# Performance work log

Hardware: AMD Instinct MI355X
Metric: run time of the kernel (lower is better)

## Reference

```python
import jax, jax.numpy as jnp
import numpy as np

B, N = 16, 4096
COORD, VAL = 2, 3
LD = 256          # latent_dim / code_dim
NC = 1024         # num_codes
HID = 256         # hidden_size
NL = 5            # num_layers
NV = 4            # num_latent_vectors (residual VQ stages)
NI = 1000         # num_images
CC = 0.25         # commitment_cost
OMEGA = 30.0


def setup_inputs() -> dict:
    key = jax.random.key(0)
    ks = jax.random.split(key, 12)
    coords = jax.random.uniform(ks[0], (B, N, COORD), jnp.float32, -1.0, 1.0)
    latent_indices = jax.random.randint(ks[1], (B,), 0, NI)
    latents = jax.random.normal(ks[2], (NI, NV, LD), jnp.float32)
    emb = jax.random.normal(ks[3], (NV, NC, LD), jnp.float32)
    emb = emb / jnp.linalg.norm(emb, axis=-1, keepdims=True)
    mod_W = jax.random.normal(ks[4], (NL, LD, 2 * HID), jnp.float32) * (1.0 / np.sqrt(LD))
    mod_b = jnp.zeros((NL, 2 * HID), jnp.float32)
    # SIREN init
    W0 = jax.random.uniform(ks[5], (COORD, HID), jnp.float32, -1.0 / COORD, 1.0 / COORD)
    b0 = jax.random.uniform(ks[6], (HID,), jnp.float32, -1.0 / np.sqrt(COORD), 1.0 / np.sqrt(COORD))
    w_bound = np.sqrt(6.0 / HID) / OMEGA
    Wh = jax.random.uniform(ks[7], (NL - 1, HID, HID), jnp.float32, -w_bound, w_bound)
    bh = jax.random.uniform(ks[8], (NL - 1, HID), jnp.float32, -1.0 / np.sqrt(HID), 1.0 / np.sqrt(HID))
    Wl = jax.random.uniform(ks[9], (HID, VAL), jnp.float32, -w_bound, w_bound)
    bl = jax.random.uniform(ks[10], (VAL,), jnp.float32, -1.0 / np.sqrt(HID), 1.0 / np.sqrt(HID))
    return {"coords": coords, "latent_indices": latent_indices, "latents": latents,
            "emb": emb, "mod_W": mod_W, "mod_b": mod_b, "W0": W0, "b0": b0,
            "Wh": Wh, "bh": bh, "Wl": Wl, "bl": bl}


def reference(coords, latent_indices, latents, emb, mod_W, mod_b, W0, b0, Wh, bh, Wl, bl):
    sg = jax.lax.stop_gradient
    # per-image latent, summed over latent vectors -> [B, LD]
    img_latents = latents[latent_indices]
    z = img_latents.sum(axis=1)
    residual = z
    z_q_sum = jnp.zeros_like(z)
    vq_loss = jnp.float32(0.0)
    for s in range(NV):  # fixed small residual-VQ stage loop
        E = emb[s]  # [NC, LD]
        # squared euclidean distances [B, NC]
        dist = (jnp.sum(residual ** 2, axis=1, keepdims=True)
                - 2.0 * residual @ E.T + jnp.sum(E ** 2, axis=1))
        idx = jnp.argmin(dist, axis=1)
        z_q = E[idx]  # [B, LD]
        z_q_st = residual + sg(z_q - residual)  # straight-through
        vq_loss = vq_loss + CC * jnp.mean((sg(z_q) - residual) ** 2)
        z_q_sum = z_q_sum + z_q_st
        residual = sg(residual - z_q_st)
    vq_loss = vq_loss / NV
    effective_z = z_q_sum  # eval: no warmup scaling
    # FiLM params per layer: [B, NL, 2*HID]
    mods = jnp.einsum('bd,ldh->blh', effective_z, mod_W) + mod_b
    gam, bet = jnp.split(mods, 2, axis=-1)  # each [B, NL, HID]
    # SIREN decoder, keeping [B, N, HID] layout
    x = jnp.sin(OMEGA * (coords @ W0 + b0))
    for i in range(1, NL):
        pre = x @ Wh[i - 1] + bh[i - 1]
        pre = pre * (1.0 + gam[:, i, None, :]) + bet[:, i, None, :]
        x = jnp.sin(OMEGA * pre)
    values = x @ Wl + bl  # [B, N, VAL]
    return values, vq_loss
```

## Files before the change

kernel.cpp:

```cpp
#include <hip/hip_runtime.h>
#include <math.h>

#define LDIM 256
#define NCODES 1024
#define HID 256
#define NLAY 5
#define NVQ 4
#define CC_ 0.25f
#define OMEGA_ 30.0f
#define BATCH 16
#define NPTS 4096
#define PTILE 64

#define WIN_OFF 4096
#define PART_OFF 4224
#define CNT_OFF 5280
#define FLAG_OFF 5288
#define FILM_OFF 8192
#define WP_BYTE 196608
#define PLANE_SHORTS (4 * 16 * 8 * 64 * 8)
#define FAST_WS_NEEDED 1245184u
#define MAGIC_ 0x13572468u

typedef __attribute__((ext_vector_type(8))) short short8;
typedef __attribute__((ext_vector_type(4))) float f32x4;

__device__ __forceinline__ unsigned int pack_split(float x) {
  unsigned int u = __builtin_bit_cast(unsigned int, x);
  float hf = __builtin_bit_cast(float, u & 0xffff0000u);
  float lf = x - hf;
  unsigned int ul = __builtin_bit_cast(unsigned int, lf);
  return (u & 0xffff0000u) | (ul >> 16);
}
__device__ __forceinline__ void split_trunc(float x, short& hi, short& lo) {
  unsigned int u = __builtin_bit_cast(unsigned int, x);
  float hf = __builtin_bit_cast(float, u & 0xffff0000u);
  float lf = x - hf;
  hi = (short)(u >> 16);
  lo = (short)(__builtin_bit_cast(unsigned int, lf) >> 16);
}
__device__ __forceinline__ float bf16_hi_f(unsigned short h) {
  return __builtin_bit_cast(float, (unsigned int)h << 16);
}
__device__ __forceinline__ unsigned int mono_u32(float f) {
  unsigned int u = __builtin_bit_cast(unsigned int, f);
  return (u & 0x80000000u) ? ~u : (u | 0x80000000u);
}

__global__ __launch_bounds__(256) void vq_prep_fused(
    const int* __restrict__ lidx,
    const float* __restrict__ latents,
    const float* __restrict__ emb,
    const float* __restrict__ Whg,
    float* __restrict__ ws, int do_prep) {
  const int blk = blockIdx.x;
  const int t = threadIdx.x;

  if (blk < 32) {
    if (!do_prep) return;
    const int li = blk >> 3;
    const int c  = blk & 7;
    const int lane = t & 63;
    const int n = lane & 15, q = lane >> 4;
    short* wp_hi = (short*)((char*)ws + WP_BYTE);
    short* wp_lo = wp_hi + PLANE_SHORTS;
    for (int h_t = (t >> 6); h_t < 16; h_t += 4) {
      short8 hv, lv;
      #pragma unroll
      for (int j = 0; j < 8; ++j) {
        float x = Whg[((size_t)(li * 256 + c * 32 + q * 8 + j)) * 256 + h_t * 16 + n];
        short hi, lo;
        split_trunc(x, hi, lo);
        hv[j] = hi; lv[j] = lo;
      }
      size_t off = ((((size_t)li * 16 + h_t) * 8 + c) * 64 + lane) * 8;
      *(short8*)&wp_hi[off] = hv;
      *(short8*)&wp_lo[off] = lv;
    }
    return;
  }

  __shared__ __align__(16) float Ech[32 * 260];
  __shared__ __align__(16) float r_s[LDIM];
  __shared__ float mval[256];
  __shared__ int   midx[256];
  __shared__ int   bcast;
  const int vqb = blk - 32;
  const int b = vqb >> 3;
  const int slice = vqb & 7;
  unsigned int* cnt  = (unsigned int*)(ws + CNT_OFF);
  unsigned int* flag = (unsigned int*)(ws + FLAG_OFF);
  unsigned long long* part = (unsigned long long*)(ws + PART_OFF);
  unsigned long long* winners = (unsigned long long*)(ws + WIN_OFF);

  if (vqb == 0 && t == 0) {
    #pragma unroll
    for (int i = 0; i < 8; ++i)
      __hip_atomic_store(&cnt[i], 0u, __ATOMIC_RELAXED, __HIP_MEMORY_SCOPE_AGENT);
    __hip_atomic_store(flag, MAGIC_, __ATOMIC_RELEASE, __HIP_MEMORY_SCOPE_AGENT);
  }

  const int ib = lidx[b];
  float z = 0.f;
  #pragma unroll
  for (int v = 0; v < NVQ; ++v) z += latents[((size_t)ib * NVQ + v) * LDIM + t];
  r_s[t] = z;
  if (slice == 0) ws[b * LDIM + t] = z;

  if (t == 0) {
    int guard = 0;
    while (__hip_atomic_load(flag, __ATOMIC_ACQUIRE, __HIP_MEMORY_SCOPE_AGENT) != MAGIC_
           && guard < (1 << 21)) { __builtin_amdgcn_s_sleep(8); ++guard; }
  }
  __syncthreads();

  const int cg = t >> 3;
  const int dq = t & 7;

  for (int s = 0; s < NVQ; ++s) {
    const float* E = emb + (size_t)s * NCODES * LDIM + (size_t)slice * 128 * LDIM;
    const float4* E4 = (const float4*)E;
    float bestv = 3.4e38f; int besti = 0;
    for (int ch = 0; ch < 4; ++ch) {
      __syncthreads();
      #pragma unroll
      for (int it = 0; it < 8; ++it) {
        int f = it * 256 + t;
        int row = f >> 6;
        int col4 = f & 63;
        *(float4*)&Ech[row * 260 + col4 * 4] = E4[(size_t)(ch * 32 + row) * 64 + col4];
      }
      __syncthreads();
      float dot = 0.f, e2 = 0.f;
      const float* er = &Ech[cg * 260];
      const float4* rr4 = (const float4*)r_s;
      #pragma unroll
      for (int j = 0; j < 8; ++j) {
        int d4 = dq + 8 * j;
        float4 e = *(const float4*)&er[d4 * 4];
        float4 rv = rr4[d4];
        dot += e.x * rv.x + e.y * rv.y + e.z * rv.z + e.w * rv.w;
        e2  += e.x * e.x + e.y * e.y + e.z * e.z + e.w * e.w;
      }
      dot += __shfl_xor(dot, 1); e2 += __shfl_xor(e2, 1);
      dot += __shfl_xor(dot, 2); e2 += __shfl_xor(e2, 2);
      dot += __shfl_xor(dot, 4); e2 += __shfl_xor(e2, 4);
      if (dq == 0) {
        float dist = e2 - 2.f * dot;
        int c = slice * 128 + ch * 32 + cg;
        if (dist < bestv) { bestv = dist; besti = c; }
      }
    }
    mval[t] = (dq == 0) ? bestv : 3.4e38f;
    midx[t] = (dq == 0) ? besti : (1 << 30);
    __syncthreads();
    for (int off = 128; off > 0; off >>= 1) {
      if (t < off) {
        float ov = mval[t + off]; int oi = midx[t + off];
        if (ov < mval[t] || (ov == mval[t] && oi < midx[t])) { mval[t] = ov; midx[t] = oi; }
      }
      __syncthreads();
    }
    if (t == 0) {
      unsigned long long pack =
          ((unsigned long long)mono_u32(mval[0]) << 32) | (unsigned int)midx[0];
      __hip_atomic_store(&part[(b * NVQ + s) * 8 + slice], pack,
                         __ATOMIC_RELAXED, __HIP_MEMORY_SCOPE_AGENT);
      __hip_atomic_fetch_add(&cnt[s], 1u, __ATOMIC_RELEASE, __HIP_MEMORY_SCOPE_AGENT);
      int guard = 0;
      while (__hip_atomic_load(&cnt[s], __ATOMIC_ACQUIRE, __HIP_MEMORY_SCOPE_AGENT) < 128u
             && guard < (1 << 21)) { __builtin_amdgcn_s_sleep(8); ++guard; }
      unsigned long long best =
          __hip_atomic_load(&part[(b * NVQ + s) * 8 + 0], __ATOMIC_RELAXED, __HIP_MEMORY_SCOPE_AGENT);
      #pragma unroll
      for (int s2 = 1; s2 < 8; ++s2) {
        unsigned long long v =
            __hip_atomic_load(&part[(b * NVQ + s) * 8 + s2], __ATOMIC_RELAXED, __HIP_MEMORY_SCOPE_AGENT);
        if (v < best) best = v;
      }
      bcast = (int)(best & 0xffffffffULL);
      if (slice == 0) winners[b * NVQ + s] = (unsigned long long)(unsigned int)bcast;
    }
    __syncthreads();
    const int w = bcast;
    r_s[t] -= emb[((size_t)s * NCODES + w) * LDIM + t];
    __syncthreads();
  }
}

__global__ __launch_bounds__(256) void film_loss(const float* __restrict__ emb,
                                                 const float* __restrict__ mod_W,
                                                 const float* __restrict__ mod_b,
                                                 float* __restrict__ ws,
                                                 float* __restrict__ loss_out) {
  __shared__ float z_s[LDIM];
  const int t = threadIdx.x;
  const unsigned long long* wsl = (const unsigned long long*)(ws + WIN_OFF);
  if (blockIdx.x == 64) {
    __shared__ float red[256];
    float acc = 0.f;
    for (int b = 0; b < BATCH; ++b) {
      float r = ws[b * LDIM + t];
      #pragma unroll
      for (int s = 0; s < NVQ; ++s) {
        int w = (int)(wsl[b * NVQ + s] & 0xffffffffULL);
        float e = emb[((size_t)s * NCODES + w) * LDIM + t];
        float d = e - r;
        acc += d * d;
        r -= e;
      }
    }
    red[t] = acc;
    __syncthreads();
    for (int off = 128; off > 0; off >>= 1) {
      if (t < off) red[t] += red[t + off];
      __syncthreads();
    }
    if (t == 0) loss_out[0] = red[0] * (CC_ / (NVQ * BATCH * LDIM));
    return;
  }
  const int li = blockIdx.x & 3;
  const int b  = blockIdx.x >> 2;
  const int l  = li + 1;
  float z = 0.f;
  #pragma unroll
  for (int s = 0; s < NVQ; ++s) {
    int w = (int)(wsl[b * NVQ + s] & 0xffffffffULL);
    z += emb[((size_t)s * NCODES + w) * LDIM + t];
  }
  z_s[t] = z;
  __syncthreads();
  float m1 = mod_b[l * 2 * HID + t];
  float m2 = mod_b[l * 2 * HID + HID + t];
  const float* Wm = mod_W + (size_t)l * LDIM * 2 * HID;
  #pragma unroll 4
  for (int d = 0; d < LDIM; ++d) {
    float zd = z_s[d];
    m1 = fmaf(zd, Wm[d * 2 * HID + t], m1);
    m2 = fmaf(zd, Wm[d * 2 * HID + HID + t], m2);
  }
  float* film = ws + FILM_OFF;
  film[((b * 4 + li) * 2 + 0) * HID + t] = 1.f + m1;
  film[((b * 4 + li) * 2 + 1) * HID + t] = m2;
}

__global__ __launch_bounds__(512) void siren_mfma_fast(
    const float* __restrict__ coords,
    const float* __restrict__ W0,
    const float* __restrict__ b0,
    const float* __restrict__ bhv,
    const float* __restrict__ Wl,
    const float* __restrict__ bl,
    const float* __restrict__ ws,
    float* __restrict__ out) {
  __shared__ short x_h[PTILE * 264];
  __shared__ short x_l[PTILE * 264];
  __shared__ float osum[PTILE * 8 * 3];
  const int tid = threadIdx.x;
  const int bp = blockIdx.x;
  const int b = bp >> 6;
  const int tile = bp & 63;
  const int pbase = b * NPTS + tile * PTILE;

  {
    const int oct = tid >> 6;
    const int p = tid & 63;
    const float c0 = coords[(size_t)(pbase + p) * 2 + 0];
    const float c1 = coords[(size_t)(pbase + p) * 2 + 1];
    const int d0 = oct * 32;
    for (int i = 0; i < 32; i += 8) {
      short8 hv, lv;
      #pragma unroll
      for (int j = 0; j < 8; ++j) {
        int d = d0 + i + j;
        float pre = fmaf(c0, W0[d], fmaf(c1, W0[HID + d], b0[d]));
        short hi, lo;
        split_trunc(__sinf(OMEGA_ * pre), hi, lo);
        hv[j] = hi; lv[j] = lo;
      }
      *(short8*)&x_h[p * 264 + d0 + i] = hv;
      *(short8*)&x_l[p * 264 + d0 + i] = lv;
    }
  }

  const int lane = tid & 63;
  const int hq = tid >> 6;
  const int hb = hq * 32;
  const int n = lane & 15;
  const int q = lane >> 4;

  const short* wp_hi = (const short*)((const char*)ws + WP_BYTE);
  const short* wp_lo = wp_hi + PLANE_SHORTS;
  const float* film = ws + FILM_OFF;

  for (int layer = 1; layer < NLAY; ++layer) {
    const int li = layer - 1;
    f32x4 acc[4][2];
    #pragma unroll
    for (int pt = 0; pt < 4; ++pt)
      #pragma unroll
      for (int ht = 0; ht < 2; ++ht)
        acc[pt][ht] = (f32x4){0.f, 0.f, 0.f, 0.f};

    __syncthreads();

    #pragma unroll 2
    for (int kc = 0; kc < HID; kc += 32) {
      const int c = kc >> 5;
      short8 Bh[2], Bl[2];
      #pragma unroll
      for (int ht = 0; ht < 2; ++ht) {
        const size_t wb = ((((size_t)li * 16 + hq * 2 + ht) * 8 + c) * 64 + lane) * 8;
        Bh[ht] = *(const short8*)&wp_hi[wb];
        Bl[ht] = *(const short8*)&wp_lo[wb];
      }
      short8 Ah[4], Al[4];
      #pragma unroll
      for (int pt = 0; pt < 4; ++pt) {
        const int xb = (pt * 16 + n) * 264 + kc + q * 8;
        Ah[pt] = *(const short8*)&x_h[xb];
        Al[pt] = *(const short8*)&x_l[xb];
      }
      #pragma unroll
      for (int ht = 0; ht < 2; ++ht)
        #pragma unroll
        for (int pt = 0; pt < 4; ++pt)
          acc[pt][ht] = __builtin_amdgcn_mfma_f32_16x16x32_bf16(Ah[pt], Bh[ht], acc[pt][ht], 0, 0, 0);
      #pragma unroll
      for (int ht = 0; ht < 2; ++ht)
        #pragma unroll
        for (int pt = 0; pt < 4; ++pt)
          acc[pt][ht] = __builtin_amdgcn_mfma_f32_16x16x32_bf16(Ah[pt], Bl[ht], acc[pt][ht], 0, 0, 0);
      #pragma unroll
      for (int ht = 0; ht < 2; ++ht)
        #pragma unroll
        for (int pt = 0; pt < 4; ++pt)
          acc[pt][ht] = __builtin_amdgcn_mfma_f32_16x16x32_bf16(Al[pt], Bh[ht], acc[pt][ht], 0, 0, 0);
    }

    __syncthreads();

    #pragma unroll
    for (int ht = 0; ht < 2; ++ht) {
      const int h = hb + ht * 16 + n;
      const float bias = bhv[li * HID + h];
      const float g1 = film[((b * 4 + li) * 2 + 0) * HID + h];
      const float bt = film[((b * 4 + li) * 2 + 1) * HID + h];
      #pragma unroll
      for (int pt = 0; pt < 4; ++pt) {
        #pragma unroll
        for (int r = 0; r < 4; ++r) {
          float pre = acc[pt][ht][r] + bias;
          pre = fmaf(pre, g1, bt);
          short hi, lo;
          split_trunc(__sinf(OMEGA_ * pre), hi, lo);
          const int row = pt * 16 + q * 4 + r;
          x_h[row * 264 + h] = hi;
          x_l[row * 264 + h] = lo;
        }
      }
    }
  }
  __syncthreads();

  {
    const int p = tid >> 3;
    const int dq = tid & 7;
    float v0 = 0.f, v1 = 0.f, v2 = 0.f;
    for (int i = 0; i < 32; ++i) {
      int d = dq * 32 + i;
      float xv = bf16_hi_f((unsigned short)x_h[p * 264 + d]) +
                 bf16_hi_f((unsigned short)x_l[p * 264 + d]);
      v0 = fmaf(xv, Wl[d * 3 + 0], v0);
      v1 = fmaf(xv, Wl[d * 3 + 1], v1);
      v2 = fmaf(xv, Wl[d * 3 + 2], v2);
    }
    osum[(p * 8 + dq) * 3 + 0] = v0;
    osum[(p * 8 + dq) * 3 + 1] = v1;
    osum[(p * 8 + dq) * 3 + 2] = v2;
  }
  __syncthreads();
  if (tid < PTILE) {
    const int p = tid;
    float v[3] = {bl[0], bl[1], bl[2]};
    #pragma unroll
    for (int dq = 0; dq < 8; ++dq)
      #pragma unroll
      for (int c = 0; c < 3; ++c) v[c] += osum[(p * 8 + dq) * 3 + c];
    size_t o = (size_t)(pbase + p) * 3;
    out[o + 0] = v[0]; out[o + 1] = v[1]; out[o + 2] = v[2];
  }
}

__global__ __launch_bounds__(512) void siren_mfma(
    const float* __restrict__ coords,
    const float* __restrict__ W0,
    const float* __restrict__ b0,
    const float* __restrict__ Whg,
    const float* __restrict__ bhv,
    const float* __restrict__ Wl,
    const float* __restrict__ bl,
    const float* __restrict__ ws,
    float* __restrict__ out) {
  __shared__ unsigned int x_u[128 * 260];
  __shared__ float osum[128 * 4 * 3];
  const int tid = threadIdx.x;
  const int bp = blockIdx.x;
  const int b = bp >> 5;
  const int tile = bp & 31;
  const int pbase = b * NPTS + tile * 128;
  {
    const int quarter = tid >> 7;
    const int p = tid & 127;
    const float c0 = coords[(size_t)(pbase + p) * 2 + 0];
    const float c1 = coords[(size_t)(pbase + p) * 2 + 1];
    const int d0 = quarter * 64;
    for (int i = 0; i < 64; i += 4) {
      unsigned int buf[4];
      #pragma unroll
      for (int j = 0; j < 4; ++j) {
        int d = d0 + i + j;
        float pre = fmaf(c0, W0[d], fmaf(c1, W0[HID + d], b0[d]));
        buf[j] = pack_split(__sinf(OMEGA_ * pre));
      }
      *(uint4*)&x_u[p * 260 + d0 + i] = *(uint4*)buf;
    }
  }
  const int lane = tid & 63;
  const int wv = tid >> 6;
  const int pg = wv & 1;
  const int hq = wv >> 1;
  const int pb = pg * 64;
  const int hb = hq * 64;
  const int n = lane & 15;
  const int q = lane >> 4;
  const float* film = ws + FILM_OFF;
  for (int layer = 1; layer < NLAY; ++layer) {
    const int li = layer - 1;
    f32x4 acc[4][4];
    #pragma unroll
    for (int pt = 0; pt < 4; ++pt)
      #pragma unroll
      for (int ht = 0; ht < 4; ++ht)
        acc[pt][ht] = (f32x4){0.f, 0.f, 0.f, 0.f};
    __syncthreads();
    for (int kc = 0; kc < HID; kc += 32) {
      short8 Bh[4], Bl[4];
      #pragma unroll
      for (int ht = 0; ht < 4; ++ht) {
        const float* wbase = Whg + ((size_t)(li * 256 + kc + q * 8)) * 256 + hb + ht * 16 + n;
        #pragma unroll
        for (int j = 0; j < 8; ++j) {
          short hi, lo;
          split_trunc(wbase[(size_t)j * 256], hi, lo);
          Bh[ht][j] = hi; Bl[ht][j] = lo;
        }
      }
      short8 ah[4], al[4];
      #pragma unroll
      for (int pt = 0; pt < 4; ++pt) {
        const uint4* ap = (const uint4*)&x_u[(pb + pt * 16 + n) * 260 + kc + q * 8];
        uint4 a0 = ap[0], a1 = ap[1];
        unsigned int aw[8] = {a0.x, a0.y, a0.z, a0.w, a1.x, a1.y, a1.z, a1.w};
        #pragma unroll
        for (int j = 0; j < 8; ++j) {
          ah[pt][j] = (short)(aw[j] >> 16);
          al[pt][j] = (short)(aw[j] & 0xffffu);
        }
      }
      #pragma unroll
      for (int ht = 0; ht < 4; ++ht)
        #pragma unroll
        for (int pt = 0; pt < 4; ++pt)
          acc[pt][ht] = __builtin_amdgcn_mfma_f32_16x16x32_bf16(ah[pt], Bh[ht], acc[pt][ht], 0, 0, 0);
      #pragma unroll
      for (int ht = 0; ht < 4; ++ht)
        #pragma unroll
        for (int pt = 0; pt < 4; ++pt)
          acc[pt][ht] = __builtin_amdgcn_mfma_f32_16x16x32_bf16(ah[pt], Bl[ht], acc[pt][ht], 0, 0, 0);
      #pragma unroll
      for (int ht = 0; ht < 4; ++ht)
        #pragma unroll
        for (int pt = 0; pt < 4; ++pt)
          acc[pt][ht] = __builtin_amdgcn_mfma_f32_16x16x32_bf16(al[pt], Bh[ht], acc[pt][ht], 0, 0, 0);
    }
    __syncthreads();
    #pragma unroll
    for (int ht = 0; ht < 4; ++ht) {
      const int h = hb + ht * 16 + n;
      const float bias = bhv[li * HID + h];
      const float g1 = film[((b * 4 + li) * 2 + 0) * HID + h];
      const float bt = film[((b * 4 + li) * 2 + 1) * HID + h];
      #pragma unroll
      for (int pt = 0; pt < 4; ++pt) {
        #pragma unroll
        for (int r = 0; r < 4; ++r) {
          float pre = acc[pt][ht][r] + bias;
          pre = fmaf(pre, g1, bt);
          x_u[(pb + pt * 16 + q * 4 + r) * 260 + h] = pack_split(__sinf(OMEGA_ * pre));
        }
      }
    }
  }
  __syncthreads();
  {
    const int p = tid >> 2;
    const int dq = tid & 3;
    float v0 = 0.f, v1 = 0.f, v2 = 0.f;
    for (int i = 0; i < 64; ++i) {
      int d = dq * 64 + i;
      unsigned int wrd = x_u[p * 260 + d];
      float xv = bf16_hi_f((unsigned short)(wrd >> 16)) +
                 bf16_hi_f((unsigned short)(wrd & 0xffffu));
      v0 = fmaf(xv, Wl[d * 3 + 0], v0);
      v1 = fmaf(xv, Wl[d * 3 + 1], v1);
      v2 = fmaf(xv, Wl[d * 3 + 2], v2);
    }
    osum[(p * 4 + dq) * 3 + 0] = v0;
    osum[(p * 4 + dq) * 3 + 1] = v1;
    osum[(p * 4 + dq) * 3 + 2] = v2;
  }
  __syncthreads();
  if (tid < 128) {
    const int p = tid;
    float v[3] = {bl[0], bl[1], bl[2]};
    #pragma unroll
    for (int dq = 0; dq < 4; ++dq)
      #pragma unroll
      for (int c = 0; c < 3; ++c) v[c] += osum[(p * 4 + dq) * 3 + c];
    size_t o = (size_t)(pbase + p) * 3;
    out[o + 0] = v[0]; out[o + 1] = v[1]; out[o + 2] = v[2];
  }
}

extern "C" void kernel_launch(void* const* d_in, const int* in_sizes, int n_in,
                              void* d_out, int out_size, void* d_ws, size_t ws_size,
                              hipStream_t stream) {
  (void)in_sizes; (void)n_in;
  const float* coords  = (const float*)d_in[0];
  const int*   lidx    = (const int*)d_in[1];
  const float* latents = (const float*)d_in[2];
  const float* emb     = (const float*)d_in[3];
  const float* mod_W   = (const float*)d_in[4];
  const float* mod_b   = (const float*)d_in[5];
  const float* W0      = (const float*)d_in[6];
  const float* b0      = (const float*)d_in[7];
  const float* Wh      = (const float*)d_in[8];
  const float* bh      = (const float*)d_in[9];
  const float* Wl      = (const float*)d_in[10];
  const float* bl      = (const float*)d_in[11];
  float* out = (float*)d_out;
  float* ws  = (float*)d_ws;
  float* loss_out = out + (out_size - 1);

  const bool fast = (ws_size >= FAST_WS_NEEDED);
  vq_prep_fused<<<160, 256, 0, stream>>>(lidx, latents, emb, Wh, ws, fast ? 1 : 0);
  film_loss<<<BATCH * 4 + 1, 256, 0, stream>>>(emb, mod_W, mod_b, ws, loss_out);
  if (fast)
    siren_mfma_fast<<<(BATCH * NPTS) / PTILE, 512, 0, stream>>>(coords, W0, b0, bh, Wl, bl, ws, out);
  else
    siren_mfma<<<(BATCH * NPTS) / 128, 512, 0, stream>>>(coords, W0, b0, Wh, bh, Wl, bl, ws, out);
}
```

Baseline: 278.4 us.

## Fuse FiLM and loss computation into VQ kernel and stage full codebook slice

Merges the film_loss kernel into the VQ search kernel so the 128 VQ blocks, after their grid-level stage barriers, compute FiLM modulation and the commitment loss directly from the per-slice partial winners, removing one kernel launch. Each stage now loads the whole 128-code slice into LDS at once instead of four 32-row chunks with barriers between them. A done counter resets the sync flags at the end. The cost is much larger LDS use per block (about 133 KB), which may limit co-residency and needs all 128 spin-waiting blocks to stay resident.

After: 258.6 us. 7.1% less time.

```diff
diff --git a/kernel.cpp b/kernel.cpp
--- a/kernel.cpp
+++ b/kernel.cpp
@@ -12,10 +12,10 @@
 #define NPTS 4096
 #define PTILE 64
 
-#define WIN_OFF 4096
 #define PART_OFF 4224
 #define CNT_OFF 5280
 #define FLAG_OFF 5288
+#define DONE_OFF 5289
 #define FILM_OFF 8192
 #define WP_BYTE 196608
 #define PLANE_SHORTS (4 * 16 * 8 * 64 * 8)
@@ -47,12 +47,16 @@
   return (u & 0x80000000u) ? ~u : (u | 0x80000000u);
 }
 
-__global__ __launch_bounds__(256) void vq_prep_fused(
+__global__ __launch_bounds__(256) void fused_pre(
     const int* __restrict__ lidx,
     const float* __restrict__ latents,
     const float* __restrict__ emb,
     const float* __restrict__ Whg,
-    float* __restrict__ ws, int do_prep) {
+    const float* __restrict__ mod_W,
+    const float* __restrict__ mod_b,
+    float* __restrict__ ws,
+    float* __restrict__ loss_out,
+    int do_prep) {
   const int blk = blockIdx.x;
   const int t = threadIdx.x;
 
@@ -80,7 +84,7 @@
     return;
   }
 
-  __shared__ __align__(16) float Ech[32 * 260];
+  __shared__ __align__(16) float Ech[128 * 260];
   __shared__ __align__(16) float r_s[LDIM];
   __shared__ float mval[256];
   __shared__ int   midx[256];
@@ -90,27 +94,28 @@
   const int slice = vqb & 7;
   unsigned int* cnt  = (unsigned int*)(ws + CNT_OFF);
   unsigned int* flag = (unsigned int*)(ws + FLAG_OFF);
+  unsigned int* done = (unsigned int*)(ws + DONE_OFF);
   unsigned long long* part = (unsigned long long*)(ws + PART_OFF);
-  unsigned long long* winners = (unsigned long long*)(ws + WIN_OFF);
 
   if (vqb == 0 && t == 0) {
     #pragma unroll
     for (int i = 0; i < 8; ++i)
       __hip_atomic_store(&cnt[i], 0u, __ATOMIC_RELAXED, __HIP_MEMORY_SCOPE_AGENT);
+    __hip_atomic_store(done, 0u, __ATOMIC_RELAXED, __HIP_MEMORY_SCOPE_AGENT);
     __hip_atomic_store(flag, MAGIC_, __ATOMIC_RELEASE, __HIP_MEMORY_SCOPE_AGENT);
   }
 
-  const int ib = lidx[b];
-  float z = 0.f;
-  #pragma unroll
-  for (int v = 0; v < NVQ; ++v) z += latents[((size_t)ib * NVQ + v) * LDIM + t];
-  r_s[t] = z;
-  if (slice == 0) ws[b * LDIM + t] = z;
-
+  {
+    const int ib = lidx[b];
+    float z = 0.f;
+    #pragma unroll
+    for (int v = 0; v < NVQ; ++v) z += latents[((size_t)ib * NVQ + v) * LDIM + t];
+    r_s[t] = z;
+  }
   if (t == 0) {
     int guard = 0;
     while (__hip_atomic_load(flag, __ATOMIC_ACQUIRE, __HIP_MEMORY_SCOPE_AGENT) != MAGIC_
-           && guard < (1 << 21)) { __builtin_amdgcn_s_sleep(8); ++guard; }
+           && guard < (1 << 22)) { __builtin_amdgcn_s_sleep(8); ++guard; }
   }
   __syncthreads();
 
@@ -120,20 +125,19 @@
   for (int s = 0; s < NVQ; ++s) {
     const float* E = emb + (size_t)s * NCODES * LDIM + (size_t)slice * 128 * LDIM;
     const float4* E4 = (const float4*)E;
+    #pragma unroll 8
+    for (int it = 0; it < 32; ++it) {
+      int row = it * 4 + (t >> 6);
+      int col4 = t & 63;
+      *(float4*)&Ech[row * 260 + col4 * 4] = E4[(size_t)row * 64 + col4];
+    }
+    __syncthreads();
     float bestv = 3.4e38f; int besti = 0;
-    for (int ch = 0; ch < 4; ++ch) {
-      __syncthreads();
-      #pragma unroll
-      for (int it = 0; it < 8; ++it) {
-        int f = it * 256 + t;
-        int row = f >> 6;
-        int col4 = f & 63;
-        *(float4*)&Ech[row * 260 + col4 * 4] = E4[(size_t)(ch * 32 + row) * 64 + col4];
-      }
-      __syncthreads();
+    for (int cp = 0; cp < 4; ++cp) {
+      const int cl = cp * 32 + cg;
+      const float* er = &Ech[cl * 260];
+      const float4* rr4 = (const float4*)r_s;
       float dot = 0.f, e2 = 0.f;
-      const float* er = &Ech[cg * 260];
-      const float4* rr4 = (const float4*)r_s;
       #pragma unroll
       for (int j = 0; j < 8; ++j) {
         int d4 = dq + 8 * j;
@@ -147,8 +151,7 @@
       dot += __shfl_xor(dot, 4); e2 += __shfl_xor(e2, 4);
       if (dq == 0) {
         float dist = e2 - 2.f * dot;
-        int c = slice * 128 + ch * 32 + cg;
-        if (dist < bestv) { bestv = dist; besti = c; }
+        if (dist < bestv) { bestv = dist; besti = slice * 128 + cl; }
       }
     }
     mval[t] = (dq == 0) ? bestv : 3.4e38f;
@@ -169,7 +172,7 @@
       __hip_atomic_fetch_add(&cnt[s], 1u, __ATOMIC_RELEASE, __HIP_MEMORY_SCOPE_AGENT);
       int guard = 0;
       while (__hip_atomic_load(&cnt[s], __ATOMIC_ACQUIRE, __HIP_MEMORY_SCOPE_AGENT) < 128u
-             && guard < (1 << 21)) { __builtin_amdgcn_s_sleep(8); ++guard; }
+             && guard < (1 << 22)) { __builtin_amdgcn_s_sleep(8); ++guard; }
       unsigned long long best =
           __hip_atomic_load(&part[(b * NVQ + s) * 8 + 0], __ATOMIC_RELAXED, __HIP_MEMORY_SCOPE_AGENT);
       #pragma unroll
@@ -179,69 +182,98 @@
         if (v < best) best = v;
       }
       bcast = (int)(best & 0xffffffffULL);
-      if (slice == 0) winners[b * NVQ + s] = (unsigned long long)(unsigned int)bcast;
-    }
-    __syncthreads();
-    const int w = bcast;
-    r_s[t] -= emb[((size_t)s * NCODES + w) * LDIM + t];
-    __syncthreads();
-  }
-}
-
-__global__ __launch_bounds__(256) void film_loss(const float* __restrict__ emb,
-                                                 const float* __restrict__ mod_W,
-                                                 const float* __restrict__ mod_b,
-                                                 float* __restrict__ ws,
-                                                 float* __restrict__ loss_out) {
-  __shared__ float z_s[LDIM];
-  const int t = threadIdx.x;
-  const unsigned long long* wsl = (const unsigned long long*)(ws + WIN_OFF);
-  if (blockIdx.x == 64) {
-    __shared__ float red[256];
+    }
+    __syncthreads();
+    if (s < NVQ - 1) r_s[t] -= emb[((size_t)s * NCODES + bcast) * LDIM + t];
+    __syncthreads();
+  }
+
+  if (vqb < 64) {
+    const int fb = vqb >> 2;
+    const int li = vqb & 3;
+    const int l  = li + 1;
+    int w[NVQ];
+    #pragma unroll
+    for (int s = 0; s < NVQ; ++s) {
+      unsigned long long best =
+          __hip_atomic_load(&part[(fb * NVQ + s) * 8 + 0], __ATOMIC_RELAXED, __HIP_MEMORY_SCOPE_AGENT);
+      #pragma unroll
+      for (int s2 = 1; s2 < 8; ++s2) {
+        unsigned long long v =
+            __hip_atomic_load(&part[(fb * NVQ + s) * 8 + s2], __ATOMIC_RELAXED, __HIP_MEMORY_SCOPE_AGENT);
+        if (v < best) best = v;
+      }
+      w[s] = (int)(best & 0xffffffffULL);
+    }
+    float z = 0.f;
+    #pragma unroll
+    for (int s = 0; s < NVQ; ++s)
+      z += emb[((size_t)s * NCODES + w[s]) * LDIM + t];
+    __syncthreads();
+    r_s[t] = z;
+    __syncthreads();
+    float m1 = mod_b[l * 2 * HID + t];
+    float m2 = mod_b[l * 2 * HID + HID + t];
+    const float* Wm = mod_W + (size_t)l * LDIM * 2 * HID;
+    #pragma unroll 4
+    for (int d = 0; d < LDIM; ++d) {
+      float zd = r_s[d];
+      m1 = fmaf(zd, Wm[d * 2 * HID + t], m1);
+      m2 = fmaf(zd, Wm[d * 2 * HID + HID + t], m2);
+    }
+    float* film = ws + FILM_OFF;
+    film[((fb * 4 + li) * 2 + 0) * HID + t] = 1.f + m1;
+    film[((fb * 4 + li) * 2 + 1) * HID + t] = m2;
+  } else if (vqb == 64) {
     float acc = 0.f;
-    for (int b = 0; b < BATCH; ++b) {
-      float r = ws[b * LDIM + t];
+    for (int bb = 0; bb < BATCH; ++bb) {
+      int w[NVQ];
       #pragma unroll
       for (int s = 0; s < NVQ; ++s) {
-        int w = (int)(wsl[b * NVQ + s] & 0xffffffffULL);
-        float e = emb[((size_t)s * NCODES + w) * LDIM + t];
+        unsigned long long best =
+            __hip_atomic_load(&part[(bb * NVQ + s) * 8 + 0], __ATOMIC_RELAXED, __HIP_MEMORY_SCOPE_AGENT);
+        #pragma unroll
+        for (int s2 = 1; s2 < 8; ++s2) {
+          unsigned long long v =
+              __hip_atomic_load(&part[(bb * NVQ + s) * 8 + s2], __ATOMIC_RELAXED, __HIP_MEMORY_SCOPE_AGENT);
+          if (v < best) best = v;
+        }
+        w[s] = (int)(best & 0xffffffffULL);
+      }
+      const int ibb = lidx[bb];
+      float r = 0.f;
+      #pragma unroll
+      for (int v = 0; v < NVQ; ++v) r += latents[((size_t)ibb * NVQ + v) * LDIM + t];
+      #pragma unroll
+      for (int s = 0; s < NVQ; ++s) {
+        float e = emb[((size_t)s * NCODES + w[s]) * LDIM + t];
         float d = e - r;
         acc += d * d;
         r -= e;
       }
     }
-    red[t] = acc;
+    __syncthreads();
+    mval[t] = acc;
     __syncthreads();
     for (int off = 128; off > 0; off >>= 1) {
-      if (t < off) red[t] += red[t + off];
+      if (t < off) mval[t] += mval[t + off];
       __syncthreads();
     }
-    if (t == 0) loss_out[0] = red[0] * (CC_ / (NVQ * BATCH * LDIM));
-    return;
-  }
-  const int li = blockIdx.x & 3;
-  const int b  = blockIdx.x >> 2;
-  const int l  = li + 1;
-  float z = 0.f;
-  #pragma unroll
-  for (int s = 0; s < NVQ; ++s) {
-    int w = (int)(wsl[b * NVQ + s] & 0xffffffffULL);
-    z += emb[((size_t)s * NCODES + w) * LDIM + t];
-  }
-  z_s[t] = z;
+    if (t == 0) loss_out[0] = mval[0] * (CC_ / (NVQ * BATCH * LDIM));
+  }
+
   __syncthreads();
-  float m1 = mod_b[l * 2 * HID + t];
-  float m2 = mod_b[l * 2 * HID + HID + t];
-  const float* Wm = mod_W + (size_t)l * LDIM * 2 * HID;
-  #pragma unroll 4
-  for (int d = 0; d < LDIM; ++d) {
-    float zd = z_s[d];
-    m1 = fmaf(zd, Wm[d * 2 * HID + t], m1);
-    m2 = fmaf(zd, Wm[d * 2 * HID + HID + t], m2);
-  }
-  float* film = ws + FILM_OFF;
-  film[((b * 4 + li) * 2 + 0) * HID + t] = 1.f + m1;
-  film[((b * 4 + li) * 2 + 1) * HID + t] = m2;
+  if (t == 0) {
+    unsigned int prev =
+        __hip_atomic_fetch_add(done, 1u, __ATOMIC_ACQ_REL, __HIP_MEMORY_SCOPE_AGENT);
+    if (prev == 127u) {
+      #pragma unroll
+      for (int i = 0; i < 8; ++i)
+        __hip_atomic_store(&cnt[i], 0u, __ATOMIC_RELAXED, __HIP_MEMORY_SCOPE_AGENT);
+      __hip_atomic_store(done, 0u, __ATOMIC_RELAXED, __HIP_MEMORY_SCOPE_AGENT);
+      __hip_atomic_store(flag, 0u, __ATOMIC_RELEASE, __HIP_MEMORY_SCOPE_AGENT);
+    }
+  }
 }
 
 __global__ __launch_bounds__(512) void siren_mfma_fast(
@@ -554,8 +586,8 @@
   float* loss_out = out + (out_size - 1);
 
   const bool fast = (ws_size >= FAST_WS_NEEDED);
-  vq_prep_fused<<<160, 256, 0, stream>>>(lidx, latents, emb, Wh, ws, fast ? 1 : 0);
-  film_loss<<<BATCH * 4 + 1, 256, 0, stream>>>(emb, mod_W, mod_b, ws, loss_out);
+  fused_pre<<<160, 256, 0, stream>>>(lidx, latents, emb, Wh, mod_W, mod_b, ws,
+                                     loss_out, fast ? 1 : 0);
   if (fast)
     siren_mfma_fast<<<(BATCH * NPTS) / PTILE, 512, 0, stream>>>(coords, W0, b0, bh, Wl, bl, ws, out);
   else
```
